# Performance work log

Measured on AMD Instinct MI355X. Metric: run time of the kernel, lower is better.

Reference implementation:

```python
import jax, jax.numpy as jnp
import numpy as np

# HeteroGNN (eval mode: dropout p is identity)
# T = num_relations = number of node types; equal contiguous blocks of n nodes per type.
T = 3
N = 12288
F_IN = 512
H = 512
C = 32


def setup_inputs() -> dict:
    key = jax.random.key(0)
    k = jax.random.split(key, 8)
    n = N // T
    x = jax.random.normal(k[0], (N, F_IN), dtype=jnp.float32)
    # dense adjacency; scale by 1/n so spmm outputs stay O(1)
    adj = jax.random.uniform(k[1], (N, N), dtype=jnp.float32) * (1.0 / n)
    # node types 1..T in contiguous equal-size blocks (sorted), matching the
    # boolean-mask split semantics of the torch forward
    node_type_mask = (1 + jnp.arange(N) // n).astype(jnp.int32)
    W_conv = jax.random.normal(k[2], (T, H, F_IN), dtype=jnp.float32) * 0.02
    b_conv = jnp.zeros((T, H), dtype=jnp.float32)
    W_sage = jax.random.normal(k[3], (T, H, H), dtype=jnp.float32) * 0.02
    b_sage = jnp.zeros((T, H), dtype=jnp.float32)
    W_lin = jax.random.normal(k[4], (C, T * H), dtype=jnp.float32) * 0.02
    b_lin = jnp.zeros((C,), dtype=jnp.float32)
    return {"x": x, "adj": adj, "node_type_mask": node_type_mask,
            "W_conv": W_conv, "b_conv": b_conv,
            "W_sage": W_sage, "b_sage": b_sage,
            "W_lin": W_lin, "b_lin": b_lin}


def reference(x, adj, node_type_mask, W_conv, b_conv, W_sage, b_sage, W_lin, b_lin):
    T_, H_, F_ = W_conv.shape
    N_ = x.shape[0]
    n = N_ // T_  # nodes per type (contiguous equal blocks by construction)

    # x_list = [x[mask==i] for i=1..T]  ->  [T, n, F]
    xs = x.reshape(T_, n, F_)
    # relation i uses adj block (type 1 rows, type i+1 cols) -> adj[:n, i*n:(i+1)*n]
    adj_b = adj[:n].reshape(n, T_, n).transpose(1, 0, 2)  # [T, n, n]

    # per-relation Linear -> ReLU (torch Linear: x @ W^T + b)
    h = jax.nn.relu(jnp.einsum('tnf,thf->tnh', xs, W_conv) + b_conv[:, None, :])
    # spmm: message aggregation per relation
    m = jnp.einsum('tij,tjh->tih', adj_b, h)  # [T, n, H]
    # sage Linear -> ReLU
    h2 = jax.nn.relu(jnp.einsum('tnh,tgh->tng', m, W_sage) + b_sage[:, None, :])
    # concat relations along feature dim: [n, T*H]
    feat = h2.transpose(1, 0, 2).reshape(n, T_ * H_)
    logits = feat @ W_lin.T + b_lin
    return jax.nn.log_softmax(logits, axis=-1)
```

## Files before the change

### kernel.cpp

```cpp
#include <hip/hip_runtime.h>

typedef __attribute__((ext_vector_type(8))) short short8;
typedef __attribute__((ext_vector_type(4))) float f32x4;

__device__ __forceinline__ unsigned short f2bf(float f) {
  union { float f; unsigned u; } v; v.f = f;
  unsigned u = v.u + 0x7fffu + ((v.u >> 16) & 1u);
  return (unsigned short)(u >> 16);
}
__device__ __forceinline__ unsigned cvtpk(float lo, float hi) {
  unsigned r;
  asm("v_cvt_pk_bf16_f32 %0, %1, %2" : "=v"(r) : "v"(lo), "v"(hi));
  return r;
}
typedef unsigned int u32;
typedef u32 __attribute__((address_space(3)))* lds_u32p;
typedef const u32 __attribute__((address_space(1)))* glob_u32p;
__device__ __forceinline__ void glds16(const unsigned short* g, unsigned short* l) {
  __builtin_amdgcn_global_load_lds((glob_u32p)(const void*)g, (lds_u32p)(void*)l,
                                   16, 0, 0);
}
__device__ __forceinline__ void cast8(const float* p, unsigned short* o) {
  float4 f0 = *(const float4*)p;
  float4 f1 = *(const float4*)(p + 4);
  uint4 w;
  w.x = cvtpk(f0.x, f0.y); w.y = cvtpk(f0.z, f0.w);
  w.z = cvtpk(f1.x, f1.y); w.w = cvtpk(f1.z, f1.w);
  *(uint4*)o = w;
}

template<int GX, int GY, int BIAS_MODE, int RELU>
__device__ __forceinline__ void gemm_body(int s,
    const unsigned short* __restrict__ Ab, const unsigned short* __restrict__ Bb,
    unsigned short* __restrict__ Cv, const float* __restrict__ biasv,
    int K, int lda, int ldb, int ldc,
    long long sA, long long sB, long long sC, int sBias,
    unsigned short* lA, unsigned short* lB)
{
  const int bx = s % GX;
  const int by = (s / GX) % GY;
  const int t  = s / (GX * GY);
  const int row0 = by * 128, col0 = bx * 128;

  const unsigned short* A = Ab + (size_t)t * sA;
  const unsigned short* B = Bb + (size_t)t * sB;
  unsigned short*       C = Cv + (size_t)t * sC;

  const int tid  = threadIdx.x;
  const int lane = tid & 63;
  const int wave = tid >> 6;
  const int wr   = wave >> 1;
  const int wc   = wave & 1;
  const int fr   = lane & 15;
  const int fk   = (lane >> 4) << 3;
  const int grow = lane >> 3;
  const int gcol = (lane & 7) << 3;

  f32x4 acc[4][4] = {};

  for (int k0 = 0; k0 < K; k0 += 64) {
    __syncthreads();
    #pragma unroll
    for (int i = 0; i < 4; ++i) {
      int seg = i * 4 + wave;
      int r   = seg * 8 + grow;
      int c   = gcol ^ ((r & 7) << 3);
      glds16(A + (size_t)(row0 + r) * lda + k0 + c, &lA[seg * 512]);
      glds16(B + (size_t)(col0 + r) * ldb + k0 + c, &lB[seg * 512]);
    }
    __syncthreads();

    #pragma unroll
    for (int kk = 0; kk < 2; ++kk) {
      short8 af[4], bv[4];
      #pragma unroll
      for (int mi = 0; mi < 4; ++mi) {
        int r = wr * 64 + mi * 16 + fr;
        af[mi] = *(const short8*)&lA[r * 64 + ((kk * 32 + fk) ^ ((r & 7) << 3))];
      }
      #pragma unroll
      for (int ni = 0; ni < 4; ++ni) {
        int r = wc * 64 + ni * 16 + fr;
        bv[ni] = *(const short8*)&lB[r * 64 + ((kk * 32 + fk) ^ ((r & 7) << 3))];
      }
      #pragma unroll
      for (int mi = 0; mi < 4; ++mi)
        #pragma unroll
        for (int ni = 0; ni < 4; ++ni)
          acc[mi][ni] = __builtin_amdgcn_mfma_f32_16x16x32_bf16(
              af[mi], bv[ni], acc[mi][ni], 0, 0, 0);
    }
  }

  const float* bias = nullptr;
  if constexpr (BIAS_MODE != 0) bias = biasv + (size_t)t * sBias;
  const int erow = (lane >> 4) << 2;
  #pragma unroll
  for (int mi = 0; mi < 4; ++mi) {
    #pragma unroll
    for (int ni = 0; ni < 4; ++ni) {
      #pragma unroll
      for (int j = 0; j < 4; ++j) {
        int row = row0 + wr * 64 + mi * 16 + erow + j;
        int col = col0 + wc * 64 + ni * 16 + fr;
        float v = acc[mi][ni][j];
        if constexpr (BIAS_MODE == 1) v += bias[row];
        if constexpr (BIAS_MODE == 2) v += bias[col];
        if constexpr (RELU) v = fmaxf(v, 0.0f);
        C[(size_t)row * ldc + col] = f2bf(v);
      }
    }
  }
}

__device__ __forceinline__ int xcd_swz(int bid, int nwg) {
  return (bid & 7) * (nwg >> 3) + (bid >> 3);
}

__global__ __launch_bounds__(256)
void cast4_kernel(const float* __restrict__ x, const float* __restrict__ Wcf,
                  const float* __restrict__ Wsf, const float* __restrict__ Wlf,
                  unsigned short* __restrict__ xbf, unsigned short* __restrict__ Wc,
                  unsigned short* __restrict__ Wsg, unsigned short* __restrict__ Wlb)
{
  const int g0 = blockIdx.x * 256 + threadIdx.x;
  if (g0 < 786432) {
    cast8(x + (size_t)g0 * 8, xbf + (size_t)g0 * 8);
  } else if (g0 < 884736) {
    int j = g0 - 786432;
    cast8(Wcf + (size_t)j * 8, Wc + (size_t)j * 8);
  } else if (g0 < 983040) {
    int j = g0 - 884736;
    cast8(Wsf + (size_t)j * 8, Wsg + (size_t)j * 8);
  } else {
    int j = g0 - 983040;
    cast8(Wlf + (size_t)j * 8, Wlb + (size_t)j * 8);
  }
}

__global__ __launch_bounds__(256)
void k_gemm1_adjcast(const unsigned short* __restrict__ Wc,
                     const unsigned short* __restrict__ xbf,
                     unsigned short* __restrict__ ht,
                     const float* __restrict__ b_conv,
                     const float* __restrict__ adj,
                     unsigned short* __restrict__ adjb)
{
  __shared__ __align__(16) unsigned short lA[128 * 64];
  __shared__ __align__(16) unsigned short lB[128 * 64];
  const int bid = blockIdx.x;
  if (bid < 384) {
    gemm_body<32, 4, 1, 1>(xcd_swz(bid, 384), Wc, xbf, ht, b_conv,
                           512, 512, 512, 4096,
                           262144LL, 2097152LL, 2097152LL, 512, lA, lB);
  } else {
    const size_t stride = (size_t)(2304 - 384) * 256;
    for (size_t i = (size_t)(bid - 384) * 256 + threadIdx.x; i < 6291456u;
         i += stride)
      cast8(adj + i * 8, adjb + i * 8);
  }
}

template<int GX, int GY, int BIAS_MODE, int RELU>
__global__ __launch_bounds__(256)
void k_gemm(const unsigned short* __restrict__ Ab,
            const unsigned short* __restrict__ Bb,
            unsigned short* __restrict__ Cv, const float* __restrict__ biasv,
            int K, int lda, int ldb, int ldc,
            long long sA, long long sB, long long sC, int sBias)
{
  __shared__ __align__(16) unsigned short lA[128 * 64];
  __shared__ __align__(16) unsigned short lB[128 * 64];
  gemm_body<GX, GY, BIAS_MODE, RELU>(
      xcd_swz(blockIdx.x, GX * GY * 3), Ab, Bb, Cv, biasv,
      K, lda, ldb, ldc, sA, sB, sC, sBias, lA, lB);
}

__global__ __launch_bounds__(256)
void head_mfma(const unsigned short* __restrict__ h2,
               const unsigned short* __restrict__ Wlb,
               const float* __restrict__ blin,
               float* __restrict__ out)
{
  __shared__ float red[4][64][8];
  const int tid  = threadIdx.x;
  const int lane = tid & 63;
  const int w    = tid >> 6;
  const int row0 = blockIdx.x * 16;
  const int fr   = lane & 15;
  const int fk   = (lane >> 4) << 3;

  f32x4 acc0 = {}, acc1 = {};
  #pragma unroll
  for (int i = 0; i < 12; ++i) {
    int ks = w * 12 + i;
    int t  = ks >> 4;
    int k  = (ks & 15) << 5;
    const unsigned short* hp =
        h2 + (size_t)t * 2097152 + (size_t)(row0 + fr) * 512 + k + fk;
    short8 af = *(const short8*)hp;
    const unsigned short* wp = Wlb + (size_t)fr * 1536 + t * 512 + k + fk;
    short8 b0 = *(const short8*)wp;
    short8 b1 = *(const short8*)(wp + 16 * 1536);
    acc0 = __builtin_amdgcn_mfma_f32_16x16x32_bf16(af, b0, acc0, 0, 0, 0);
    acc1 = __builtin_amdgcn_mfma_f32_16x16x32_bf16(af, b1, acc1, 0, 0, 0);
  }

  *(f32x4*)&red[w][lane][0] = acc0;
  *(f32x4*)&red[w][lane][4] = acc1;
  __syncthreads();

  if (w == 0) {
    #pragma unroll
    for (int q = 1; q < 4; ++q) {
      acc0 += *(const f32x4*)&red[q][lane][0];
      acc1 += *(const f32x4*)&red[q][lane][4];
    }
    const float b0 = blin[fr], b1 = blin[16 + fr];
    #pragma unroll
    for (int j = 0; j < 4; ++j) {
      float v0 = acc0[j] + b0;
      float v1 = acc1[j] + b1;
      float mx = fmaxf(v0, v1);
      #pragma unroll
      for (int s2 = 1; s2 <= 8; s2 <<= 1) mx = fmaxf(mx, __shfl_xor(mx, s2, 64));
      float e = expf(v0 - mx) + expf(v1 - mx);
      #pragma unroll
      for (int s2 = 1; s2 <= 8; s2 <<= 1) e += __shfl_xor(e, s2, 64);
      float ls = mx + logf(e);
      int r = row0 + ((lane >> 4) << 2) + j;
      out[(size_t)r * 32 + fr]      = v0 - ls;
      out[(size_t)r * 32 + 16 + fr] = v1 - ls;
    }
  }
}

extern "C" void kernel_launch(void* const* d_in, const int* in_sizes, int n_in,
                              void* d_out, int out_size, void* d_ws, size_t ws_size,
                              hipStream_t stream)
{
  const float* x      = (const float*)d_in[0];
  const float* adj    = (const float*)d_in[1];
  const float* W_conv = (const float*)d_in[3];
  const float* b_conv = (const float*)d_in[4];
  const float* W_sage = (const float*)d_in[5];
  const float* b_sage = (const float*)d_in[6];
  const float* W_lin  = (const float*)d_in[7];
  const float* b_lin  = (const float*)d_in[8];
  float* out = (float*)d_out;

  unsigned short* ws   = (unsigned short*)d_ws;
  unsigned short* adjb = ws;
  unsigned short* xbf  = adjb + 50331648;
  unsigned short* Wc   = xbf  + 6291456;
  unsigned short* Wsg  = Wc   + 786432;
  unsigned short* Wlb  = Wsg  + 786432;
  unsigned short* ht   = Wlb  + 49152;
  unsigned short* m_   = ht   + 6291456;
  unsigned short* h2   = ht;

  cast4_kernel<<<3864, 256, 0, stream>>>(x, W_conv, W_sage, W_lin,
                                         xbf, Wc, Wsg, Wlb);

  k_gemm1_adjcast<<<2304, 256, 0, stream>>>(Wc, xbf, ht, b_conv, adj, adjb);

  k_gemm<4, 32, 0, 0><<<384, 256, 0, stream>>>(
      adjb, ht, m_, nullptr, 4096, 12288, 4096, 512,
      4096LL, 2097152LL, 2097152LL, 0);

  k_gemm<4, 32, 2, 1><<<384, 256, 0, stream>>>(
      m_, Wsg, h2, b_sage, 512, 512, 512, 512,
      2097152LL, 262144LL, 2097152LL, 512);

  head_mfma<<<256, 256, 0, stream>>>(h2, Wlb, b_lin, out);
}
```

Measured before the change: 188.5 us.

## Fuse fp32-to-bf16 casts of x and W_conv into first GEMM tile loads

The first GEMM now reads x and W_conv as fp32 directly, converts them to bf16 in registers and stores them into swizzled LDS, so the standalone cast kernel and its bf16 scratch buffers go away. The W_sage and W_lin casts move into the adjacency-cast blocks of the same launch. This saves one kernel launch and a round trip through global memory for the cast inputs. In exchange the GEMM tile loads become synchronous register loads instead of async global-to-LDS copies, and each weight tile is re-read and re-converted by every block that uses it.

```diff
diff --git a/kernel.cpp b/kernel.cpp
--- a/kernel.cpp
+++ b/kernel.cpp
@@ -29,9 +29,9 @@
   *(uint4*)o = w;
 }
 
-template<int GX, int GY, int BIAS_MODE, int RELU>
+template<int GX, int GY, int A_F32, int B_F32, int BIAS_MODE, int RELU>
 __device__ __forceinline__ void gemm_body(int s,
-    const unsigned short* __restrict__ Ab, const unsigned short* __restrict__ Bb,
+    const void* __restrict__ Av, const void* __restrict__ Bv,
     unsigned short* __restrict__ Cv, const float* __restrict__ biasv,
     int K, int lda, int ldb, int ldc,
     long long sA, long long sB, long long sC, int sBias,
@@ -42,9 +42,11 @@
   const int t  = s / (GX * GY);
   const int row0 = by * 128, col0 = bx * 128;
 
-  const unsigned short* A = Ab + (size_t)t * sA;
-  const unsigned short* B = Bb + (size_t)t * sB;
-  unsigned short*       C = Cv + (size_t)t * sC;
+  const unsigned short* Ab = (const unsigned short*)Av + (size_t)t * sA;
+  const float*          Af = (const float*)Av + (size_t)t * sA;
+  const unsigned short* Bb = (const unsigned short*)Bv + (size_t)t * sB;
+  const float*          Bf = (const float*)Bv + (size_t)t * sB;
+  unsigned short*       C  = Cv + (size_t)t * sC;
 
   const int tid  = threadIdx.x;
   const int lane = tid & 63;
@@ -55,18 +57,58 @@
   const int fk   = (lane >> 4) << 3;
   const int grow = lane >> 3;
   const int gcol = (lane & 7) << 3;
+  const int srow = tid >> 1;
+  const int scol = (tid & 1) << 5;
 
   f32x4 acc[4][4] = {};
 
   for (int k0 = 0; k0 < K; k0 += 64) {
     __syncthreads();
-    #pragma unroll
-    for (int i = 0; i < 4; ++i) {
-      int seg = i * 4 + wave;
-      int r   = seg * 8 + grow;
-      int c   = gcol ^ ((r & 7) << 3);
-      glds16(A + (size_t)(row0 + r) * lda + k0 + c, &lA[seg * 512]);
-      glds16(B + (size_t)(col0 + r) * ldb + k0 + c, &lB[seg * 512]);
+    if constexpr (A_F32) {
+      const float* p = Af + (size_t)(row0 + srow) * lda + k0 + scol;
+      float4 f[8];
+      #pragma unroll
+      for (int j = 0; j < 8; ++j) f[j] = *(const float4*)(p + j * 4);
+      #pragma unroll
+      for (int j = 0; j < 4; ++j) {
+        uint4 w;
+        w.x = cvtpk(f[2*j].x,   f[2*j].y);
+        w.y = cvtpk(f[2*j].z,   f[2*j].w);
+        w.z = cvtpk(f[2*j+1].x, f[2*j+1].y);
+        w.w = cvtpk(f[2*j+1].z, f[2*j+1].w);
+        *(uint4*)&lA[srow * 64 + ((scol + j * 8) ^ ((srow & 7) << 3))] = w;
+      }
+    } else {
+      #pragma unroll
+      for (int i = 0; i < 4; ++i) {
+        int seg = i * 4 + wave;
+        int r   = seg * 8 + grow;
+        glds16(Ab + (size_t)(row0 + r) * lda + k0 + (gcol ^ ((r & 7) << 3)),
+               &lA[seg * 512]);
+      }
+    }
+    if constexpr (B_F32) {
+      const float* p = Bf + (size_t)(col0 + srow) * ldb + k0 + scol;
+      float4 f[8];
+      #pragma unroll
+      for (int j = 0; j < 8; ++j) f[j] = *(const float4*)(p + j * 4);
+      #pragma unroll
+      for (int j = 0; j < 4; ++j) {
+        uint4 w;
+        w.x = cvtpk(f[2*j].x,   f[2*j].y);
+        w.y = cvtpk(f[2*j].z,   f[2*j].w);
+        w.z = cvtpk(f[2*j+1].x, f[2*j+1].y);
+        w.w = cvtpk(f[2*j+1].z, f[2*j+1].w);
+        *(uint4*)&lB[srow * 64 + ((scol + j * 8) ^ ((srow & 7) << 3))] = w;
+      }
+    } else {
+      #pragma unroll
+      for (int i = 0; i < 4; ++i) {
+        int seg = i * 4 + wave;
+        int r   = seg * 8 + grow;
+        glds16(Bb + (size_t)(col0 + r) * ldb + k0 + (gcol ^ ((r & 7) << 3)),
+               &lB[seg * 512]);
+      }
     }
     __syncthreads();
 
@@ -118,46 +160,33 @@
 }
 
 __global__ __launch_bounds__(256)
-void cast4_kernel(const float* __restrict__ x, const float* __restrict__ Wcf,
-                  const float* __restrict__ Wsf, const float* __restrict__ Wlf,
-                  unsigned short* __restrict__ xbf, unsigned short* __restrict__ Wc,
-                  unsigned short* __restrict__ Wsg, unsigned short* __restrict__ Wlb)
-{
-  const int g0 = blockIdx.x * 256 + threadIdx.x;
-  if (g0 < 786432) {
-    cast8(x + (size_t)g0 * 8, xbf + (size_t)g0 * 8);
-  } else if (g0 < 884736) {
-    int j = g0 - 786432;
-    cast8(Wcf + (size_t)j * 8, Wc + (size_t)j * 8);
-  } else if (g0 < 983040) {
-    int j = g0 - 884736;
-    cast8(Wsf + (size_t)j * 8, Wsg + (size_t)j * 8);
-  } else {
-    int j = g0 - 983040;
-    cast8(Wlf + (size_t)j * 8, Wlb + (size_t)j * 8);
-  }
-}
-
-__global__ __launch_bounds__(256)
-void k_gemm1_adjcast(const unsigned short* __restrict__ Wc,
-                     const unsigned short* __restrict__ xbf,
-                     unsigned short* __restrict__ ht,
-                     const float* __restrict__ b_conv,
-                     const float* __restrict__ adj,
-                     unsigned short* __restrict__ adjb)
+void k_gemm1_casts(const float* __restrict__ W_conv, const float* __restrict__ x,
+                   unsigned short* __restrict__ ht, const float* __restrict__ b_conv,
+                   const float* __restrict__ adj, unsigned short* __restrict__ adjb,
+                   const float* __restrict__ Wsf, unsigned short* __restrict__ Wsg,
+                   const float* __restrict__ Wlf, unsigned short* __restrict__ Wlb)
 {
   __shared__ __align__(16) unsigned short lA[128 * 64];
   __shared__ __align__(16) unsigned short lB[128 * 64];
   const int bid = blockIdx.x;
   if (bid < 384) {
-    gemm_body<32, 4, 1, 1>(xcd_swz(bid, 384), Wc, xbf, ht, b_conv,
-                           512, 512, 512, 4096,
-                           262144LL, 2097152LL, 2097152LL, 512, lA, lB);
+    gemm_body<32, 4, 1, 1, 1, 1>(xcd_swz(bid, 384), W_conv, x, ht, b_conv,
+                                 512, 512, 512, 4096,
+                                 262144LL, 2097152LL, 2097152LL, 512, lA, lB);
   } else {
     const size_t stride = (size_t)(2304 - 384) * 256;
-    for (size_t i = (size_t)(bid - 384) * 256 + threadIdx.x; i < 6291456u;
-         i += stride)
-      cast8(adj + i * 8, adjb + i * 8);
+    for (size_t i = (size_t)(bid - 384) * 256 + threadIdx.x; i < 6395904u;
+         i += stride) {
+      if (i < 6291456u) {
+        cast8(adj + i * 8, adjb + i * 8);
+      } else if (i < 6389760u) {
+        size_t j = i - 6291456u;
+        cast8(Wsf + j * 8, Wsg + j * 8);
+      } else {
+        size_t j = i - 6389760u;
+        cast8(Wlf + j * 8, Wlb + j * 8);
+      }
+    }
   }
 }
 
@@ -171,7 +200,7 @@
 {
   __shared__ __align__(16) unsigned short lA[128 * 64];
   __shared__ __align__(16) unsigned short lB[128 * 64];
-  gemm_body<GX, GY, BIAS_MODE, RELU>(
+  gemm_body<GX, GY, 0, 0, BIAS_MODE, RELU>(
       xcd_swz(blockIdx.x, GX * GY * 3), Ab, Bb, Cv, biasv,
       K, lda, ldb, ldc, sA, sB, sC, sBias, lA, lB);
 }
@@ -251,18 +280,14 @@
 
   unsigned short* ws   = (unsigned short*)d_ws;
   unsigned short* adjb = ws;
-  unsigned short* xbf  = adjb + 50331648;
-  unsigned short* Wc   = xbf  + 6291456;
-  unsigned short* Wsg  = Wc   + 786432;
+  unsigned short* Wsg  = adjb + 50331648;
   unsigned short* Wlb  = Wsg  + 786432;
   unsigned short* ht   = Wlb  + 49152;
   unsigned short* m_   = ht   + 6291456;
   unsigned short* h2   = ht;
 
-  cast4_kernel<<<3864, 256, 0, stream>>>(x, W_conv, W_sage, W_lin,
-                                         xbf, Wc, Wsg, Wlb);
-
-  k_gemm1_adjcast<<<2304, 256, 0, stream>>>(Wc, xbf, ht, b_conv, adj, adjb);
+  k_gemm1_casts<<<2304, 256, 0, stream>>>(W_conv, x, ht, b_conv,
+                                          adj, adjb, W_sage, Wsg, W_lin, Wlb);
 
   k_gemm<4, 32, 0, 0><<<384, 256, 0, stream>>>(
       adjb, ht, m_, nullptr, 4096, 12288, 4096, 512,
```

After: 201.5 us. +6.9%, slower.

## Split adjacency cast and spmm K-range to overlap second-half cast with first-half spmm

Applied to the files above, without the earlier changes.

The fp32-to-bf16 cast of the adjacency block is split into two halves along K. The first half is cast alongside the first GEMM. The second half is cast in the same launch as an spmm over the first K half, which writes fp32 partial sums. A final spmm over the second K half adds those partials before storing bf16. This hides part of the cast's memory traffic behind spmm compute, at the cost of an extra fp32 partial buffer write and read plus one more launch.

```diff
diff --git a/kernel.cpp b/kernel.cpp
--- a/kernel.cpp
+++ b/kernel.cpp
@@ -29,10 +29,11 @@
   *(uint4*)o = w;
 }
 
-template<int GX, int GY, int BIAS_MODE, int RELU>
+template<int GX, int GY, int BIAS_MODE, int RELU, int CMODE>
 __device__ __forceinline__ void gemm_body(int s,
     const unsigned short* __restrict__ Ab, const unsigned short* __restrict__ Bb,
-    unsigned short* __restrict__ Cv, const float* __restrict__ biasv,
+    void* __restrict__ Cw, const float* __restrict__ biasv,
+    const float* __restrict__ Pacc,
     int K, int lda, int ldb, int ldc,
     long long sA, long long sB, long long sC, int sBias,
     unsigned short* lA, unsigned short* lB)
@@ -42,9 +43,10 @@
   const int t  = s / (GX * GY);
   const int row0 = by * 128, col0 = bx * 128;
 
-  const unsigned short* A = Ab + (size_t)t * sA;
-  const unsigned short* B = Bb + (size_t)t * sB;
-  unsigned short*       C = Cv + (size_t)t * sC;
+  const unsigned short* A  = Ab + (size_t)t * sA;
+  const unsigned short* B  = Bb + (size_t)t * sB;
+  unsigned short*       C  = (unsigned short*)Cw + (size_t)t * sC;
+  float*                Cf = (float*)Cw + (size_t)t * sC;
 
   const int tid  = threadIdx.x;
   const int lane = tid & 63;
@@ -107,7 +109,14 @@
         if constexpr (BIAS_MODE == 1) v += bias[row];
         if constexpr (BIAS_MODE == 2) v += bias[col];
         if constexpr (RELU) v = fmaxf(v, 0.0f);
-        C[(size_t)row * ldc + col] = f2bf(v);
+        if constexpr (CMODE == 1) {
+          Cf[(size_t)row * ldc + col] = v;
+        } else if constexpr (CMODE == 2) {
+          v += Pacc[(size_t)t * sC + (size_t)row * ldc + col];
+          C[(size_t)row * ldc + col] = f2bf(v);
+        } else {
+          C[(size_t)row * ldc + col] = f2bf(v);
+        }
       }
     }
   }
@@ -139,40 +148,67 @@
 }
 
 __global__ __launch_bounds__(256)
-void k_gemm1_adjcast(const unsigned short* __restrict__ Wc,
-                     const unsigned short* __restrict__ xbf,
-                     unsigned short* __restrict__ ht,
-                     const float* __restrict__ b_conv,
-                     const float* __restrict__ adj,
-                     unsigned short* __restrict__ adjb)
+void k_gemm1_cast1(const unsigned short* __restrict__ Wc,
+                   const unsigned short* __restrict__ xbf,
+                   unsigned short* __restrict__ ht,
+                   const float* __restrict__ b_conv,
+                   const float* __restrict__ adj,
+                   unsigned short* __restrict__ adjb)
 {
   __shared__ __align__(16) unsigned short lA[128 * 64];
   __shared__ __align__(16) unsigned short lB[128 * 64];
   const int bid = blockIdx.x;
   if (bid < 384) {
-    gemm_body<32, 4, 1, 1>(xcd_swz(bid, 384), Wc, xbf, ht, b_conv,
-                           512, 512, 512, 4096,
-                           262144LL, 2097152LL, 2097152LL, 512, lA, lB);
+    gemm_body<32, 4, 1, 1, 0>(xcd_swz(bid, 384), Wc, xbf, ht, b_conv, nullptr,
+                              512, 512, 512, 4096,
+                              262144LL, 2097152LL, 2097152LL, 512, lA, lB);
   } else {
-    const size_t stride = (size_t)(2304 - 384) * 256;
-    for (size_t i = (size_t)(bid - 384) * 256 + threadIdx.x; i < 6291456u;
-         i += stride)
-      cast8(adj + i * 8, adjb + i * 8);
-  }
-}
-
-template<int GX, int GY, int BIAS_MODE, int RELU>
+    const size_t stride = (size_t)(2048 - 384) * 256;
+    for (size_t q = (size_t)(bid - 384) * 256 + threadIdx.x; q < 3145728u;
+         q += stride) {
+      size_t g = (q >> 8) * 512 + (q & 255);
+      cast8(adj + g * 8, adjb + g * 8);
+    }
+  }
+}
+
+__global__ __launch_bounds__(256)
+void k_spmm1_cast2(const unsigned short* __restrict__ adjb,
+                   const unsigned short* __restrict__ ht,
+                   float* __restrict__ m1f,
+                   const float* __restrict__ adj,
+                   unsigned short* __restrict__ adjb_w)
+{
+  __shared__ __align__(16) unsigned short lA[128 * 64];
+  __shared__ __align__(16) unsigned short lB[128 * 64];
+  const int bid = blockIdx.x;
+  if (bid < 384) {
+    gemm_body<4, 32, 0, 0, 1>(xcd_swz(bid, 384), adjb, ht, (void*)m1f, nullptr,
+                              nullptr, 2048, 12288, 4096, 512,
+                              4096LL, 2097152LL, 2097152LL, 0, lA, lB);
+  } else {
+    const size_t stride = (size_t)(2048 - 384) * 256;
+    for (size_t q = (size_t)(bid - 384) * 256 + threadIdx.x; q < 3145728u;
+         q += stride) {
+      size_t g = (q >> 8) * 512 + 256 + (q & 255);
+      cast8(adj + g * 8, adjb_w + g * 8);
+    }
+  }
+}
+
+template<int GX, int GY, int BIAS_MODE, int RELU, int CMODE>
 __global__ __launch_bounds__(256)
 void k_gemm(const unsigned short* __restrict__ Ab,
             const unsigned short* __restrict__ Bb,
-            unsigned short* __restrict__ Cv, const float* __restrict__ biasv,
+            void* __restrict__ Cw, const float* __restrict__ biasv,
+            const float* __restrict__ Pacc,
             int K, int lda, int ldb, int ldc,
             long long sA, long long sB, long long sC, int sBias)
 {
   __shared__ __align__(16) unsigned short lA[128 * 64];
   __shared__ __align__(16) unsigned short lB[128 * 64];
-  gemm_body<GX, GY, BIAS_MODE, RELU>(
-      xcd_swz(blockIdx.x, GX * GY * 3), Ab, Bb, Cv, biasv,
+  gemm_body<GX, GY, BIAS_MODE, RELU, CMODE>(
+      xcd_swz(blockIdx.x, GX * GY * 3), Ab, Bb, Cw, biasv, Pacc,
       K, lda, ldb, ldc, sA, sB, sC, sBias, lA, lB);
 }
 
@@ -257,20 +293,23 @@
   unsigned short* Wlb  = Wsg  + 786432;
   unsigned short* ht   = Wlb  + 49152;
   unsigned short* m_   = ht   + 6291456;
+  float*          m1f  = (float*)(m_ + 6291456);
   unsigned short* h2   = ht;
 
   cast4_kernel<<<3864, 256, 0, stream>>>(x, W_conv, W_sage, W_lin,
                                          xbf, Wc, Wsg, Wlb);
 
-  k_gemm1_adjcast<<<2304, 256, 0, stream>>>(Wc, xbf, ht, b_conv, adj, adjb);
-
-  k_gemm<4, 32, 0, 0><<<384, 256, 0, stream>>>(
-      adjb, ht, m_, nullptr, 4096, 12288, 4096, 512,
-      4096LL, 2097152LL, 2097152LL, 0);
-
-  k_gemm<4, 32, 2, 1><<<384, 256, 0, stream>>>(
-      m_, Wsg, h2, b_sage, 512, 512, 512, 512,
-      2097152LL, 262144LL, 2097152LL, 512);
+  k_gemm1_cast1<<<2048, 256, 0, stream>>>(Wc, xbf, ht, b_conv, adj, adjb);
+
+  k_spmm1_cast2<<<2048, 256, 0, stream>>>(adjb, ht, m1f, adj, adjb);
+
+  k_gemm<4, 32, 0, 0, 2><<<384, 256, 0, stream>>>(
+      adjb + 2048, ht + 2048, m_, nullptr, m1f,
+      2048, 12288, 4096, 512, 4096LL, 2097152LL, 2097152LL, 0);
+
+  k_gemm<4, 32, 2, 1, 0><<<384, 256, 0, stream>>>(
+      m_, Wsg, h2, b_sage, nullptr,
+      512, 512, 512, 512, 2097152LL, 262144LL, 2097152LL, 512);
 
   head_mfma<<<256, 256, 0, stream>>>(h2, Wlb, b_lin, out);
 }
```

New measurement: 189.9 us. About the same (+0.7%).
